# Kernel optimization log

Hardware: AMD Instinct MI355X
Metric: run time of the kernel (lower is better)

## Reference

```python
import jax, jax.numpy as jnp
import numpy as np

BS = 8
LEVEL = 128.0 / 255.0

RGB2YCC = jnp.array([[0.299, 0.587, 0.114],
                     [-0.168735892, -0.331264108, 0.5],
                     [0.5, -0.418687589, -0.081312411]], dtype=jnp.float32)
YCC2RGB = jnp.array([[1.0, 0.0, 1.402],
                     [1.0, -0.344136286, -0.714136286],
                     [1.0, 1.772, 0.0]], dtype=jnp.float32)


def _dctmtx(bs=BS):
    i = np.arange(bs)[:, None]
    j = np.arange(bs)[None, :]
    m = np.sqrt(2.0 / bs) * np.cos(np.pi * (2 * j + 1) * i / (2 * bs))
    m[0, :] = 1.0 / np.sqrt(bs)
    return jnp.asarray(m, dtype=jnp.float32)

DCT = _dctmtx()


def _blockify(x, bs=BS):
    # [B,H,W] -> [B,H/bs,W/bs,bs,bs]
    B, H, W = x.shape
    return x.reshape(B, H // bs, bs, W // bs, bs).transpose(0, 1, 3, 2, 4)


def _deblockify(x):
    B, hb, wb, bs, _ = x.shape
    return x.transpose(0, 1, 3, 2, 4).reshape(B, hb * bs, wb * bs)


def _round_ste(x):
    return x + jax.lax.stop_gradient(jnp.round(x) - x)


def _clamp_ste(x, lo, hi):
    return x + jax.lax.stop_gradient(jnp.clip(x, lo, hi) - x)


def setup_inputs() -> dict:
    key = jax.random.key(0)
    k1, k2 = jax.random.split(key)
    inp = jax.random.uniform(k1, (32, 3, 512, 512), dtype=jnp.float32)
    quantize = jax.random.uniform(k2, (3, BS, BS), dtype=jnp.float32,
                                  minval=40.0 / 255.0, maxval=50.0 / 255.0)
    return {"input": inp, "quantize": quantize}


def reference(input, quantize):
    B, _, H, W = input.shape
    off = jnp.array([0.0, LEVEL, LEVEL], dtype=jnp.float32)[None, :, None, None]

    # RGB -> YCbCr (plain clamp), then level shift -128/255 on all channels
    ycc = jnp.einsum('bchw,kc->bkhw', input, RGB2YCC)
    ycc = jnp.clip(ycc + off, 0.0, 1.0) - LEVEL

    # chroma 4:2:0 subsample: 2x2 mean pooling
    y = ycc[:, 0]
    cb = ycc[:, 1].reshape(B, H // 2, 2, W // 2, 2).mean(axis=(2, 4))
    cr = ycc[:, 2].reshape(B, H // 2, 2, W // 2, 2).mean(axis=(2, 4))

    # Faithful: eval path uses rounded qtable; quantize[0] used for ALL channels
    qtable = jnp.round(quantize[0] * 255.0) / 255.0

    def codec(ch):
        blk = _blockify(ch)                      # [B,hb,wb,8,8]
        d = DCT @ blk @ DCT.T                    # blockwise 2D DCT
        dec = _round_ste(d / qtable) * qtable    # straight-through quantize
        idct = DCT.T @ dec @ DCT                 # blockwise 2D IDCT
        return _deblockify(idct)

    y2, cb2, cr2 = codec(y), codec(cb), codec(cr)

    up = lambda c: jnp.repeat(jnp.repeat(c, 2, axis=1), 2, axis=2)
    ycc2 = jnp.stack([y2, up(cb2), up(cr2)], axis=1) + LEVEL

    # YCbCr -> RGB: subtract 128/255 from chroma only, matmul, STE clamp
    ycc2 = ycc2 - off
    rgb = jnp.einsum('bchw,kc->bkhw', ycc2, YCC2RGB)
    return _clamp_ste(rgb, 0.0, 1.0)
```

## Files before the change

### kernel.cpp

```cpp
#include <hip/hip_runtime.h>
#include <cmath>


#define LEVELD 0.5019607843137255
#define LEVELF 0.5019607843137255f
#define BAND   5.0e-5f

#define CA  0.35355339059327373f
#define CB0 0.49039264020161522f
#define CB1 0.41573480615127262f
#define CB2 0.27778511650980114f
#define CB3 0.09754516100806413f
#define CC0 0.46193976625564337f
#define CC1 0.19134171618254489f

__device__ const double DMATD[64] = {
  0.3535533905932738,  0.3535533905932738,  0.3535533905932738,  0.3535533905932738,
  0.3535533905932738,  0.3535533905932738,  0.3535533905932738,  0.3535533905932738,
  0.4903926402016152,  0.4157348061512726,  0.2777851165098011,  0.0975451610080641,
 -0.0975451610080641, -0.2777851165098011, -0.4157348061512726, -0.4903926402016152,
  0.4619397662556434,  0.1913417161825449, -0.1913417161825449, -0.4619397662556434,
 -0.4619397662556434, -0.1913417161825449,  0.1913417161825449,  0.4619397662556434,
  0.4157348061512726, -0.0975451610080641, -0.4903926402016152, -0.2777851165098011,
  0.2777851165098011,  0.4903926402016152,  0.0975451610080641, -0.4157348061512726,
  0.3535533905932738, -0.3535533905932738, -0.3535533905932738,  0.3535533905932738,
  0.3535533905932738, -0.3535533905932738, -0.3535533905932738,  0.3535533905932738,
  0.2777851165098011, -0.4903926402016152,  0.0975451610080641,  0.4157348061512726,
 -0.4157348061512726, -0.0975451610080641,  0.4903926402016152, -0.2777851165098011,
  0.1913417161825449, -0.4619397662556434,  0.4619397662556434, -0.1913417161825449,
 -0.1913417161825449,  0.4619397662556434, -0.4619397662556434,  0.1913417161825449,
  0.0975451610080641, -0.2777851165098011,  0.4157348061512726, -0.4903926402016152,
  0.4903926402016152, -0.4157348061512726,  0.2777851165098011, -0.0975451610080641
};

__device__ __forceinline__ float dpp_xor1(float x) {
  return __int_as_float(__builtin_amdgcn_mov_dpp(__float_as_int(x), 0xB1, 0xF, 0xF, true));
}
__device__ __forceinline__ float dpp_xor2(float x) {
  return __int_as_float(__builtin_amdgcn_mov_dpp(__float_as_int(x), 0x4E, 0xF, 0xF, true));
}
__device__ __forceinline__ float dpp_xor4(float x) {
  int t = __builtin_amdgcn_mov_dpp(__float_as_int(x), 0x141, 0xF, 0xF, true);
  return __int_as_float(__builtin_amdgcn_mov_dpp(t, 0x1B, 0xF, 0xF, true));
}

__device__ __forceinline__ void transpose8(float v[8], int p) {
  { float t[8];
    #pragma unroll
    for (int j = 0; j < 8; ++j) t[j] = dpp_xor1(v[j ^ 1]);
    const bool lb = (p & 1) != 0;
    #pragma unroll
    for (int j = 0; j < 8; ++j) v[j] = (lb == ((j & 1) != 0)) ? v[j] : t[j];
  }
  { float t[8];
    #pragma unroll
    for (int j = 0; j < 8; ++j) t[j] = dpp_xor2(v[j ^ 2]);
    const bool lb = (p & 2) != 0;
    #pragma unroll
    for (int j = 0; j < 8; ++j) v[j] = (lb == ((j & 2) != 0)) ? v[j] : t[j];
  }
  { float t[8];
    #pragma unroll
    for (int j = 0; j < 8; ++j) t[j] = dpp_xor4(v[j ^ 4]);
    const bool lb = (p & 4) != 0;
    #pragma unroll
    for (int j = 0; j < 8; ++j) v[j] = (lb == ((j & 4) != 0)) ? v[j] : t[j];
  }
}

__device__ __forceinline__ void fdct8b(float x[8]) {
  const float s0 = x[0] + x[7], s1 = x[1] + x[6], s2 = x[2] + x[5], s3 = x[3] + x[4];
  const float d0 = x[0] - x[7], d1 = x[1] - x[6], d2 = x[2] - x[5], d3 = x[3] - x[4];
  const float t0 = s0 + s3, t1 = s1 + s2, t2 = s0 - s3, t3 = s1 - s2;
  x[0] = CA * (t0 + t1);
  x[4] = CA * (t0 - t1);
  x[2] = fmaf(CC0, t2,  CC1 * t3);
  x[6] = fmaf(CC1, t2, -CC0 * t3);
  x[1] = fmaf(CB0, d0, fmaf( CB1, d1, fmaf( CB2, d2,  CB3 * d3)));
  x[3] = fmaf(CB1, d0, fmaf(-CB3, d1, fmaf(-CB0, d2, -CB2 * d3)));
  x[5] = fmaf(CB2, d0, fmaf(-CB0, d1, fmaf( CB3, d2,  CB1 * d3)));
  x[7] = fmaf(CB3, d0, fmaf(-CB2, d1, fmaf( CB1, d2, -CB0 * d3)));
}
__device__ __forceinline__ void idct8b(float y[8]) {
  const float pe = CA * (y[0] + y[4]), qe = CA * (y[0] - y[4]);
  const float re = fmaf(CC0, y[2],  CC1 * y[6]);
  const float se = fmaf(CC1, y[2], -CC0 * y[6]);
  const float E0 = pe + re, E3 = pe - re, E1 = qe + se, E2 = qe - se;
  const float O0 = fmaf(CB0, y[1], fmaf( CB1, y[3], fmaf( CB2, y[5],  CB3 * y[7])));
  const float O1 = fmaf(CB1, y[1], fmaf(-CB3, y[3], fmaf(-CB0, y[5], -CB2 * y[7])));
  const float O2 = fmaf(CB2, y[1], fmaf(-CB0, y[3], fmaf( CB3, y[5],  CB1 * y[7])));
  const float O3 = fmaf(CB3, y[1], fmaf(-CB2, y[3], fmaf( CB1, y[5], -CB0 * y[7])));
  y[0] = E0 + O0; y[7] = E0 - O0;
  y[1] = E1 + O1; y[6] = E1 - O1;
  y[2] = E2 + O2; y[5] = E2 - O2;
  y[3] = E3 + O3; y[4] = E3 - O3;
}

__device__ __attribute__((noinline)) float rescue_coef(
    const float* __restrict__ quant, const float* __restrict__ base,
    int mode, int i, int j)
{
  double acc = 0.0;
  if (mode == 0) {
    #pragma unroll 1
    for (int k = 0; k < 8; ++k) {
      double e = 0.0;
      #pragma unroll
      for (int l = 0; l < 8; ++l) {
        const size_t off = (size_t)k * 512 + l;
        const double rr = (double)base[off];
        const double gg = (double)base[262144 + off];
        const double bb = (double)base[524288 + off];
        double y = 0.299 * rr + 0.587 * gg + 0.114 * bb;
        y = fmin(fmax(y, 0.0), 1.0) - LEVELD;
        e += y * DMATD[j * 8 + l];
      }
      acc += DMATD[i * 8 + k] * e;
    }
  } else {
    const double c0 = (mode == 1) ? -0.168735892 : 0.5;
    const double c1 = (mode == 1) ? -0.331264108 : -0.418687589;
    const double c2 = (mode == 1) ?  0.5         : -0.081312411;
    #pragma unroll 1
    for (int k = 0; k < 8; ++k) {
      double e = 0.0;
      #pragma unroll 1
      for (int l = 0; l < 8; ++l) {
        double m = 0.0;
        #pragma unroll
        for (int dr = 0; dr < 2; ++dr)
          #pragma unroll
          for (int dc = 0; dc < 2; ++dc) {
            const size_t off = (size_t)(2 * k + dr) * 512 + (2 * l + dc);
            const double rr = (double)base[off];
            const double gg = (double)base[262144 + off];
            const double bb = (double)base[524288 + off];
            const double v = c0 * rr + c1 * gg + c2 * bb;
            m += fmin(fmax(v + LEVELD, 0.0), 1.0) - LEVELD;
          }
        e += (0.25 * m) * DMATD[j * 8 + l];
      }
      acc += DMATD[i * 8 + k] * e;
    }
  }
  const double qd = rint((double)quant[i * 8 + j] * 255.0) * (1.0 / 255.0);
  return (float)(rint(acc / qd) * qd);
}

__device__ __forceinline__ void codec8(float x[8], const float qv[8], const float rq[8],
                                       int p, int mode, const float* __restrict__ base,
                                       const float* __restrict__ quant)
{
  fdct8b(x); transpose8(x, p); fdct8b(x);
  unsigned bad = 0u;
  #pragma unroll
  for (int i = 0; i < 8; ++i) {
    const float tt = x[i] * rq[i];
    const float rt = rintf(tt);
    if (fabsf(tt - rt) > 0.5f - BAND) bad |= (1u << i);
    x[i] = rt * qv[i];
  }
  if (__builtin_expect(bad != 0u, 0)) {
    do {
      const int i = __builtin_ctz(bad);
      bad &= bad - 1u;
      const float fix = rescue_coef(quant, base, mode, i, p);
      #pragma unroll
      for (int k = 0; k < 8; ++k) x[k] = (k == i) ? fix : x[k];
    } while (bad != 0u);
  }
  idct8b(x); transpose8(x, p); idct8b(x);
}

__device__ __forceinline__ void color_stage(
    const float4 L6[6], int tY, int qr, int qc, int p,
    float4* __restrict__ CHW, float rout[8])
{
  const float RL[8] = {L6[0].x, L6[0].y, L6[0].z, L6[0].w, L6[1].x, L6[1].y, L6[1].z, L6[1].w};
  const float GL[8] = {L6[2].x, L6[2].y, L6[2].z, L6[2].w, L6[3].x, L6[3].y, L6[3].z, L6[3].w};
  const float BL[8] = {L6[4].x, L6[4].y, L6[4].z, L6[4].w, L6[5].x, L6[5].y, L6[5].z, L6[5].w};

  float cbv[8], crv[8];
  #pragma unroll
  for (int l = 0; l < 8; ++l) {
    const float rr = RL[l], gg = GL[l], bb = BL[l];
    const float y  = fmaf(0.114f, bb, fmaf(0.587f, gg, 0.299f * rr));
    const float cb = fmaf(0.5f, bb, fmaf(-0.331264108f, gg, -0.168735892f * rr));
    const float cr = fmaf(-0.081312411f, bb, fmaf(-0.418687589f, gg, 0.5f * rr));
    rout[l] = fminf(fmaxf(y,           0.0f), 1.0f) - LEVELF;
    cbv[l]  = fminf(fmaxf(cb + LEVELF, 0.0f), 1.0f) - LEVELF;
    crv[l]  = fminf(fmaxf(cr + LEVELF, 0.0f), 1.0f) - LEVELF;
  }
  float ch[4];
  #pragma unroll
  for (int j = 0; j < 4; ++j) {
    const float cbh = cbv[2 * j] + cbv[2 * j + 1];
    const float crh = crv[2 * j] + crv[2 * j + 1];
    const float cbs = cbh + dpp_xor1(cbh);
    const float crs = crh + dpp_xor1(crh);
    ch[j] = 0.25f * ((p & 1) ? crs : cbs);
  }
  const int crow = qr * 4 + (p >> 1);
  const int slot = ((((p & 1) * 4 + tY) * 16) + crow * 2 + qc) ^ ((tY << 1) | qr);
  CHW[slot] = make_float4(ch[0], ch[1], ch[2], ch[3]);
}

__device__ __forceinline__ void out_phase(
    float* __restrict__ ob, int tY, int qr, int qc, int p,
    const float4* __restrict__ CHW, const float r[8])
{
  const int crow = qr * 4 + (p >> 1);
  const int swz = (tY << 1) | qr;
  const float4 cb4 = CHW[((tY * 16) + crow * 2 + qc) ^ swz];
  const float4 cr4 = CHW[(((4 + tY) * 16) + crow * 2 + qc) ^ swz];
  const float cba[4] = {cb4.x, cb4.y, cb4.z, cb4.w};
  const float cra[4] = {cr4.x, cr4.y, cr4.z, cr4.w};

  float RR[8], GG[8], BB[8];
  #pragma unroll
  for (int l = 0; l < 8; ++l) {
    const float y2 = r[l] + LEVELF;
    const float cbb = cba[l >> 1], crr = cra[l >> 1];
    float ro = fmaf(1.402f, crr, y2);
    float go = y2 - 0.344136286f * cbb - 0.714136286f * crr;
    float bo = fmaf(1.772f, cbb, y2);
    RR[l] = fminf(fmaxf(ro, 0.0f), 1.0f);
    GG[l] = fminf(fmaxf(go, 0.0f), 1.0f);
    BB[l] = fminf(fmaxf(bo, 0.0f), 1.0f);
  }
  float* op = ob + (size_t)(qr * 8 + p) * 512 + tY * 16 + qc * 8;
  *(float4*)(op)              = make_float4(RR[0], RR[1], RR[2], RR[3]);
  *(float4*)(op + 4)          = make_float4(RR[4], RR[5], RR[6], RR[7]);
  *(float4*)(op + 262144)     = make_float4(GG[0], GG[1], GG[2], GG[3]);
  *(float4*)(op + 262148)     = make_float4(GG[4], GG[5], GG[6], GG[7]);
  *(float4*)(op + 524288)     = make_float4(BB[0], BB[1], BB[2], BB[3]);
  *(float4*)(op + 524292)     = make_float4(BB[4], BB[5], BB[6], BB[7]);
}

__global__ __launch_bounds__(128, 4) void jpeg_fused(
    const float* __restrict__ in, const float* __restrict__ quant,
    float* __restrict__ out)
{
  __shared__ float4 CH[2][128];

  const int wv   = threadIdx.x >> 6;
  const int lane = threadIdx.x & 63;
  const int g = lane >> 3, p = lane & 7;
  const int tx = g >> 2, qr = (g >> 1) & 1, qc = g & 1;

  const int u    = blockIdx.x * 2 + wv;
  const int img  = u >> 8;
  const int trow = (u >> 3) & 31;
  const int tcq  = u & 7;
  const size_t tboff = (size_t)img * 786432 + (size_t)trow * 16 * 512 + (size_t)tcq * 64;
  const float* tb = in + tboff;
  float* ob = out + tboff;
  float4* CHW = &CH[wv][0];

  float4 L[2][6];
  #pragma unroll
  for (int h = 0; h < 2; ++h) {
    const int tY = 2 * h + tx;
    const float* pb = tb + (size_t)(qr * 8 + p) * 512 + tY * 16 + qc * 8;
    L[h][0] = *(const float4*)(pb);
    L[h][1] = *(const float4*)(pb + 4);
    L[h][2] = *(const float4*)(pb + 262144);
    L[h][3] = *(const float4*)(pb + 262148);
    L[h][4] = *(const float4*)(pb + 524288);
    L[h][5] = *(const float4*)(pb + 524292);
  }
  float qf[8];
  #pragma unroll
  for (int i = 0; i < 8; ++i) qf[i] = quant[i * 8 + p];

  float qv[8], rq[8];
  #pragma unroll
  for (int i = 0; i < 8; ++i) {
    qv[i] = rintf(qf[i] * 255.0f) * (1.0f / 255.0f);
    rq[i] = 1.0f / qv[i];
  }

  float rA[8], rB[8];
  color_stage(L[0], 2 * 0 + tx, qr, qc, p, CHW, rA);
  color_stage(L[1], 2 * 1 + tx, qr, qc, p, CHW, rB);
  __builtin_amdgcn_wave_barrier();

  const float* blkA = tb + (size_t)(qr * 8) * 512 + (2 * 0 + tx) * 16 + qc * 8;
  const float* blkB = tb + (size_t)(qr * 8) * 512 + (2 * 1 + tx) * 16 + qc * 8;
  codec8(rA, qv, rq, p, 0, blkA, quant);
  codec8(rB, qv, rq, p, 0, blkB, quant);

  {
    const int cpar = g >> 2, ct = g & 3;
    const int pre  = (cpar * 4 + ct) * 16 + p * 2;
    const int swz  = (ct << 1) | (p >> 2);
    const int sl = pre ^ swz, sh = (pre + 1) ^ swz;
    const float4 a = CHW[sl];
    const float4 b = CHW[sh];
    float xc[8] = {a.x, a.y, a.z, a.w, b.x, b.y, b.z, b.w};
    codec8(xc, qv, rq, p, 1 + cpar, tb + ct * 16, quant);
    CHW[sl] = make_float4(xc[0], xc[1], xc[2], xc[3]);
    CHW[sh] = make_float4(xc[4], xc[5], xc[6], xc[7]);
  }
  __builtin_amdgcn_wave_barrier();

  out_phase(ob, 2 * 0 + tx, qr, qc, p, CHW, rA);
  out_phase(ob, 2 * 1 + tx, qr, qc, p, CHW, rB);
}

extern "C" void kernel_launch(void* const* d_in, const int* in_sizes, int n_in,
                              void* d_out, int out_size, void* d_ws, size_t ws_size,
                              hipStream_t stream) {
  const float* in    = (const float*)d_in[0];
  const float* quant = (const float*)d_in[1];
  float* out = (float*)d_out;

  jpeg_fused<<<dim3(4096), dim3(128), 0, stream>>>(in, quant, out);
}
```

Measured before the change: 66.27 us.

## Make waves persistent over four units with register double-buffered prefetch

Each wave now processes four tile units, strided eight images apart, in a loop and prefetches the next unit's RGB pixels into registers while the DCT codec of the current unit runs. Blocks grow to 256 threads and the grid shrinks to 512 blocks, and the quantization table is computed once per wave instead of once per unit. The aim is to hide global-load latency behind compute and to amortize launch and setup cost. In exchange, register pressure rises and fewer blocks are available to hide latency through occupancy.

```diff
diff --git a/kernel.cpp b/kernel.cpp
--- a/kernel.cpp
+++ b/kernel.cpp
@@ -172,8 +172,23 @@
   idct8b(x); transpose8(x, p); idct8b(x);
 }
 
+__device__ __forceinline__ void load_unit(const float* __restrict__ tb,
+                                          size_t lanerow, float4 P[12])
+{
+  #pragma unroll
+  for (int h = 0; h < 2; ++h) {
+    const float* pb = tb + lanerow + h * 32;
+    P[6 * h + 0] = *(const float4*)(pb);
+    P[6 * h + 1] = *(const float4*)(pb + 4);
+    P[6 * h + 2] = *(const float4*)(pb + 262144);
+    P[6 * h + 3] = *(const float4*)(pb + 262148);
+    P[6 * h + 4] = *(const float4*)(pb + 524288);
+    P[6 * h + 5] = *(const float4*)(pb + 524292);
+  }
+}
+
 __device__ __forceinline__ void color_stage(
-    const float4 L6[6], int tY, int qr, int qc, int p,
+    const float4* __restrict__ L6, int tY, int qr, int qc, int p,
     float4* __restrict__ CHW, float rout[8])
 {
   const float RL[8] = {L6[0].x, L6[0].y, L6[0].z, L6[0].w, L6[1].x, L6[1].y, L6[1].z, L6[1].w};
@@ -237,75 +252,74 @@
   *(float4*)(op + 524292)     = make_float4(BB[4], BB[5], BB[6], BB[7]);
 }
 
-__global__ __launch_bounds__(128, 4) void jpeg_fused(
+#define UNIT_STRIDE 6291456
+
+__global__ __launch_bounds__(256, 2) void jpeg_fused(
     const float* __restrict__ in, const float* __restrict__ quant,
     float* __restrict__ out)
 {
-  __shared__ float4 CH[2][128];
+  __shared__ float4 CH[4][128];
 
   const int wv   = threadIdx.x >> 6;
   const int lane = threadIdx.x & 63;
   const int g = lane >> 3, p = lane & 7;
   const int tx = g >> 2, qr = (g >> 1) & 1, qc = g & 1;
 
-  const int u    = blockIdx.x * 2 + wv;
-  const int img  = u >> 8;
-  const int trow = (u >> 3) & 31;
-  const int tcq  = u & 7;
-  const size_t tboff = (size_t)img * 786432 + (size_t)trow * 16 * 512 + (size_t)tcq * 64;
-  const float* tb = in + tboff;
-  float* ob = out + tboff;
+  const int wave_id = blockIdx.x * 4 + wv;
+  const int img0 = wave_id >> 8;
+  const int trow = (wave_id >> 3) & 31;
+  const int tcq  = wave_id & 7;
+  const size_t base0 = (size_t)img0 * 786432 + (size_t)trow * 8192 + (size_t)tcq * 64;
   float4* CHW = &CH[wv][0];
 
-  float4 L[2][6];
-  #pragma unroll
-  for (int h = 0; h < 2; ++h) {
-    const int tY = 2 * h + tx;
-    const float* pb = tb + (size_t)(qr * 8 + p) * 512 + tY * 16 + qc * 8;
-    L[h][0] = *(const float4*)(pb);
-    L[h][1] = *(const float4*)(pb + 4);
-    L[h][2] = *(const float4*)(pb + 262144);
-    L[h][3] = *(const float4*)(pb + 262148);
-    L[h][4] = *(const float4*)(pb + 524288);
-    L[h][5] = *(const float4*)(pb + 524292);
-  }
-  float qf[8];
-  #pragma unroll
-  for (int i = 0; i < 8; ++i) qf[i] = quant[i * 8 + p];
+  const size_t lanerow = (size_t)(qr * 8 + p) * 512 + tx * 16 + qc * 8;
 
   float qv[8], rq[8];
   #pragma unroll
   for (int i = 0; i < 8; ++i) {
-    qv[i] = rintf(qf[i] * 255.0f) * (1.0f / 255.0f);
+    qv[i] = rintf(quant[i * 8 + p] * 255.0f) * (1.0f / 255.0f);
     rq[i] = 1.0f / qv[i];
   }
 
-  float rA[8], rB[8];
-  color_stage(L[0], 2 * 0 + tx, qr, qc, p, CHW, rA);
-  color_stage(L[1], 2 * 1 + tx, qr, qc, p, CHW, rB);
-  __builtin_amdgcn_wave_barrier();
-
-  const float* blkA = tb + (size_t)(qr * 8) * 512 + (2 * 0 + tx) * 16 + qc * 8;
-  const float* blkB = tb + (size_t)(qr * 8) * 512 + (2 * 1 + tx) * 16 + qc * 8;
-  codec8(rA, qv, rq, p, 0, blkA, quant);
-  codec8(rB, qv, rq, p, 0, blkB, quant);
-
-  {
-    const int cpar = g >> 2, ct = g & 3;
-    const int pre  = (cpar * 4 + ct) * 16 + p * 2;
-    const int swz  = (ct << 1) | (p >> 2);
-    const int sl = pre ^ swz, sh = (pre + 1) ^ swz;
-    const float4 a = CHW[sl];
-    const float4 b = CHW[sh];
-    float xc[8] = {a.x, a.y, a.z, a.w, b.x, b.y, b.z, b.w};
-    codec8(xc, qv, rq, p, 1 + cpar, tb + ct * 16, quant);
-    CHW[sl] = make_float4(xc[0], xc[1], xc[2], xc[3]);
-    CHW[sh] = make_float4(xc[4], xc[5], xc[6], xc[7]);
-  }
-  __builtin_amdgcn_wave_barrier();
-
-  out_phase(ob, 2 * 0 + tx, qr, qc, p, CHW, rA);
-  out_phase(ob, 2 * 1 + tx, qr, qc, p, CHW, rB);
+  float4 P[12];
+  load_unit(in + base0, lanerow, P);
+
+  #pragma unroll 1
+  for (int k = 0; k < 4; ++k) {
+    const float* tb_cur = in + base0 + (size_t)k * UNIT_STRIDE;
+    float* ob = out + base0 + (size_t)k * UNIT_STRIDE;
+
+    float rA[8], rB[8];
+    color_stage(&P[0], 0 + tx, qr, qc, p, CHW, rA);
+    color_stage(&P[6], 2 + tx, qr, qc, p, CHW, rB);
+    __builtin_amdgcn_wave_barrier();
+
+    if (k < 3) load_unit(tb_cur + UNIT_STRIDE, lanerow, P);
+    __builtin_amdgcn_sched_barrier(0);
+
+    const float* blkA = tb_cur + (size_t)qr * 4096 + (0 + tx) * 16 + qc * 8;
+    const float* blkB = tb_cur + (size_t)qr * 4096 + (2 + tx) * 16 + qc * 8;
+    codec8(rA, qv, rq, p, 0, blkA, quant);
+    codec8(rB, qv, rq, p, 0, blkB, quant);
+
+    {
+      const int cpar = g >> 2, ct = g & 3;
+      const int pre  = (cpar * 4 + ct) * 16 + p * 2;
+      const int swz  = (ct << 1) | (p >> 2);
+      const int sl = pre ^ swz, sh = (pre + 1) ^ swz;
+      const float4 a = CHW[sl];
+      const float4 b = CHW[sh];
+      float xc[8] = {a.x, a.y, a.z, a.w, b.x, b.y, b.z, b.w};
+      codec8(xc, qv, rq, p, 1 + cpar, tb_cur + ct * 16, quant);
+      CHW[sl] = make_float4(xc[0], xc[1], xc[2], xc[3]);
+      CHW[sh] = make_float4(xc[4], xc[5], xc[6], xc[7]);
+    }
+    __builtin_amdgcn_wave_barrier();
+
+    out_phase(ob, 0 + tx, qr, qc, p, CHW, rA);
+    out_phase(ob, 2 + tx, qr, qc, p, CHW, rB);
+    __builtin_amdgcn_wave_barrier();
+  }
 }
 
 extern "C" void kernel_launch(void* const* d_in, const int* in_sizes, int n_in,
@@ -315,5 +329,5 @@
   const float* quant = (const float*)d_in[1];
   float* out = (float*)d_out;
 
-  jpeg_fused<<<dim3(4096), dim3(128), 0, stream>>>(in, quant, out);
-}
+  jpeg_fused<<<dim3(512), dim3(256), 0, stream>>>(in, quant, out);
+}
```

After: 78.55 us, median of 2. 18.5% more time.
